# Kernel optimization log

Hardware: AMD Instinct MI355X
Metric: run time of the kernel (lower is better)

## Reference

```python
import jax, jax.numpy as jnp
import numpy as np

COST_CLASS = 1.0
COST_MASK = 1.0
COST_DICE = 1.0


def setup_inputs() -> dict:
    key = jax.random.key(0)
    k1, k2, k3, k4 = jax.random.split(key, 4)
    B, Q, T, H, W, C = 4, 100, 20, 128, 128, 80
    out_probs = jax.random.normal(k1, (B, Q, C), dtype=jnp.float32)
    out_masks = jax.random.uniform(k2, (B, Q, H, W), dtype=jnp.float32)
    target_masks = jax.random.uniform(k3, (B, T, H, W), dtype=jnp.float32)
    target_labels = jax.random.randint(k4, (B, T), 0, C, dtype=jnp.int64)
    return {"out_probs": out_probs, "out_masks": out_masks,
            "target_masks": target_masks, "target_labels": target_labels}


def reference(out_probs, out_masks, target_masks, target_labels):
    # out_probs: [B,Q,C]; out_masks: [B,Q,H,W]; target_masks: [B,T,H,W]; target_labels: [B,T]
    B, Q = out_probs.shape[:2]
    T = target_labels.shape[1]

    # Classification cost: -softmax(out_probs)[b, q, target_labels[b, t]] -> [B,Q,T]
    prob = jax.nn.softmax(out_probs, axis=-1)
    idx = jnp.broadcast_to(target_labels[:, None, :], (B, Q, T))
    cost_class = -jnp.take_along_axis(prob, idx, axis=2)

    out_flat = out_masks.reshape(B, Q, -1)      # [B,Q,HW]
    tgt_flat = target_masks.reshape(B, T, -1)   # [B,T,HW]

    # Pairwise L1 cost over pixels: [B,Q,T]
    cost_mask = jnp.abs(out_flat[:, :, None, :] - tgt_flat[:, None, :, :]).sum(-1)

    # Pairwise dice cost: numerator via batched matmul, sums broadcast.
    inter = jnp.einsum('bqn,btn->bqt', out_flat, tgt_flat)
    denom = out_flat.sum(-1)[:, :, None] + tgt_flat.sum(-1)[:, None, :]
    cost_dice = 1.0 - (2.0 * inter + 1.0) / (denom + 1.0)

    C_mat = COST_MASK * cost_mask + COST_CLASS * cost_class + COST_DICE * cost_dice
    return C_mat  # [B,Q,T] cost matrix (Hungarian assignment runs on CPU outside)
```

## Files before the change

### kernel.cpp

```cpp
#include <hip/hip_runtime.h>
#include <hip/hip_bf16.h>
#include <math.h>

#define B_ 4
#define Q_ 100
#define T_ 20
#define C_ 80
#define HW_ 16384

#define S_ 8
#define QP_ (Q_ / 2)
#define SEG4_ (HW_ / S_ / 4)
#define NIT_ (SEG4_ / 64)
#define TW_ 5

#define NBLK_ (B_ * QP_ * S_)
#define WL_OFF 0
#define WI_OFF (NBLK_ * 40)
#define OS_OFF (WI_OFF + NBLK_ * 40)
#define GS_OFF (OS_OFF + NBLK_ * 2)

typedef float f32x4 __attribute__((ext_vector_type(4)));

__device__ __forceinline__ float wred(float v) {
    v += __shfl_down(v, 32);
    v += __shfl_down(v, 16);
    v += __shfl_down(v, 8);
    v += __shfl_down(v, 4);
    v += __shfl_down(v, 2);
    v += __shfl_down(v, 1);
    return v;
}

template <bool WITH_G>
__device__ __forceinline__ void partial_body(const f32x4* __restrict__ o4,
                                             const f32x4* __restrict__ g4,
                                             float* __restrict__ ws,
                                             int blin, int b, int seg,
                                             int lane, int ts) {
    const int t0 = ts * TW_;

    float accL[2][TW_], accI[2][TW_], os[2], gs[TW_];
#pragma unroll
    for (int qi = 0; qi < 2; ++qi) {
        os[qi] = 0.f;
#pragma unroll
        for (int tj = 0; tj < TW_; ++tj) { accL[qi][tj] = 0.f; accI[qi][tj] = 0.f; }
    }
#pragma unroll
    for (int tj = 0; tj < TW_; ++tj) gs[tj] = 0.f;

#pragma unroll
    for (int it = 0; it < NIT_; ++it) {
        const int ofs = it * 64;
        const f32x4 o0 = o4[ofs];
        const f32x4 o1 = o4[(HW_ / 4) + ofs];
        os[0] += (o0.x + o0.y) + (o0.z + o0.w);
        os[1] += (o1.x + o1.y) + (o1.z + o1.w);
#pragma unroll
        for (int tj = 0; tj < TW_; ++tj) {
            const f32x4 g = g4[(size_t)(t0 + tj) * (HW_ / 4) + ofs];
            if (WITH_G) gs[tj] += (g.x + g.y) + (g.z + g.w);
            accL[0][tj] += (fabsf(o0.x - g.x) + fabsf(o0.y - g.y)) +
                           (fabsf(o0.z - g.z) + fabsf(o0.w - g.w));
            accI[0][tj] = fmaf(o0.x, g.x, accI[0][tj]);
            accI[0][tj] = fmaf(o0.y, g.y, accI[0][tj]);
            accI[0][tj] = fmaf(o0.z, g.z, accI[0][tj]);
            accI[0][tj] = fmaf(o0.w, g.w, accI[0][tj]);
            accL[1][tj] += (fabsf(o1.x - g.x) + fabsf(o1.y - g.y)) +
                           (fabsf(o1.z - g.z) + fabsf(o1.w - g.w));
            accI[1][tj] = fmaf(o1.x, g.x, accI[1][tj]);
            accI[1][tj] = fmaf(o1.y, g.y, accI[1][tj]);
            accI[1][tj] = fmaf(o1.z, g.z, accI[1][tj]);
            accI[1][tj] = fmaf(o1.w, g.w, accI[1][tj]);
        }
    }

    float* WL = ws + WL_OFF;
    float* WI = ws + WI_OFF;
    float* OS = ws + OS_OFF;
    float* GS = ws + GS_OFF;
#pragma unroll
    for (int qi = 0; qi < 2; ++qi) {
#pragma unroll
        for (int tj = 0; tj < TW_; ++tj) {
            const float vL = wred(accL[qi][tj]);
            const float vI = wred(accI[qi][tj]);
            if (lane == 0) {
                WL[(blin * 4 + ts) * 10 + qi * TW_ + tj] = vL;
                WI[(blin * 4 + ts) * 10 + qi * TW_ + tj] = vI;
            }
        }
        const float vo = wred(os[qi]);
        if (ts == 0 && lane == 0) OS[blin * 2 + qi] = vo;
    }
    if (WITH_G) {
#pragma unroll
        for (int tj = 0; tj < TW_; ++tj) {
            const float vg = wred(gs[tj]);
            if (lane == 0) GS[(b * S_ + seg) * T_ + t0 + tj] = vg;
        }
    }
}

__global__ __launch_bounds__(256) void partial_kernel(const float* __restrict__ outm,
                                                      const float* __restrict__ tgtm,
                                                      float* __restrict__ ws) {
    const int r = blockIdx.x & 7;
    const int m = blockIdx.x >> 3;
    const int b = r >> 1;
    const int l = m * 2 + (r & 1);
    const int qp = l >> 3;
    const int seg = l & (S_ - 1);
    const int blin = (b * QP_ + qp) * S_ + seg;

    const int lane = threadIdx.x & 63;
    const int ts   = threadIdx.x >> 6;

    const f32x4* o4 = (const f32x4*)(outm + ((size_t)b * Q_ + qp * 2) * HW_) + seg * SEG4_ + lane;
    const f32x4* g4 = (const f32x4*)(tgtm + (size_t)b * T_ * HW_) + seg * SEG4_ + lane;

    if (qp == 0) partial_body<true>(o4, g4, ws, blin, b, seg, lane, ts);
    else         partial_body<false>(o4, g4, ws, blin, b, seg, lane, ts);
}

__global__ __launch_bounds__(64) void finalize_kernel(const float* __restrict__ probs,
                                                      const int*   __restrict__ labels,
                                                      const float* __restrict__ ws,
                                                      float* __restrict__ out) {
    const int bq = blockIdx.x;
    const int b = bq / Q_;
    const int q = bq % Q_;
    const int qp = q >> 1;
    const int qi = q & 1;

    __shared__ float s_logit[C_];
    for (int c = threadIdx.x; c < C_; c += 64)
        s_logit[c] = probs[(size_t)bq * C_ + c];
    __syncthreads();

    const float* WL = ws + WL_OFF;
    const float* WI = ws + WI_OFF;
    const float* OS = ws + OS_OFF;
    const float* GS = ws + GS_OFF;

    const int t = threadIdx.x;
    if (t < T_) {
        const int ts = t / TW_, tj = t % TW_;
        float L = 0.f, I = 0.f, osum = 0.f, tsum = 0.f;
#pragma unroll
        for (int seg = 0; seg < S_; ++seg) {
            const int blin = (b * QP_ + qp) * S_ + seg;
            L    += WL[(blin * 4 + ts) * 10 + qi * TW_ + tj];
            I    += WI[(blin * 4 + ts) * 10 + qi * TW_ + tj];
            osum += OS[blin * 2 + qi];
            tsum += GS[(b * S_ + seg) * T_ + t];
        }
        float mx = -INFINITY;
#pragma unroll
        for (int c = 0; c < C_; ++c) mx = fmaxf(mx, s_logit[c]);
        float sum = 0.f;
#pragma unroll
        for (int c = 0; c < C_; ++c) sum += __expf(s_logit[c] - mx);
        const int lab = labels[b * T_ + t];
        const float p = __expf(s_logit[lab] - mx) / sum;

        const float denom = osum + tsum;
        const float dice = 1.f - (2.f * I + 1.f) / (denom + 1.f);

        out[(size_t)bq * T_ + t] = L - p + dice;
    }
}

extern "C" void kernel_launch(void* const* d_in, const int* in_sizes, int n_in,
                              void* d_out, int out_size, void* d_ws, size_t ws_size,
                              hipStream_t stream) {
    const float* out_probs     = (const float*)d_in[0];
    const float* out_masks     = (const float*)d_in[1];
    const float* target_masks  = (const float*)d_in[2];
    const int*   target_labels = (const int*)d_in[3];
    float* out = (float*)d_out;

    float* partials = (float*)d_ws;

    partial_kernel<<<B_ * QP_ * S_, 256, 0, stream>>>(out_masks, target_masks, partials);
    finalize_kernel<<<B_ * Q_, 64, 0, stream>>>(out_probs, target_labels, partials, out);
}
```

Measured before the change: 35.60 us.

## Widen query tile to ten per block and shorten cross-lane reductions

Each block now processes 10 queries against 5 targets per wave instead of 2, so every loaded target vector is reused across more queries. The pixel range is split into 16 segments rather than 8, giving 640 blocks instead of 1600. Warp reductions stop at 4 lanes, and the finalize kernel adds the 4 partials per cell with float4 loads. The aim is to cut redundant target-mask reads and reduction shuffles. The cost is far more accumulator registers (about 100 floats plus 15 loaded vectors), which risks lower occupancy or spills, and fewer blocks to spread across the GPU.

New measurement: 62.94 us. 1.77x slower.

```diff
diff --git a/kernel.cpp b/kernel.cpp
--- a/kernel.cpp
+++ b/kernel.cpp
@@ -8,41 +8,38 @@
 #define C_ 80
 #define HW_ 16384
 
-#define S_ 8
-#define QP_ (Q_ / 2)
+#define S_ 16
+#define QG_ 10
+#define NQG_ (Q_ / QG_)
+#define TW_ 5
 #define SEG4_ (HW_ / S_ / 4)
 #define NIT_ (SEG4_ / 64)
-#define TW_ 5
 
-#define NBLK_ (B_ * QP_ * S_)
-#define WL_OFF 0
-#define WI_OFF (NBLK_ * 40)
-#define OS_OFF (WI_OFF + NBLK_ * 40)
-#define GS_OFF (OS_OFF + NBLK_ * 2)
+#define CELL_ 1640
+#define NCELL_ (B_ * NQG_ * S_)
+#define GS_OFF ((size_t)NCELL_ * CELL_)
 
 typedef float f32x4 __attribute__((ext_vector_type(4)));
 
-__device__ __forceinline__ float wred(float v) {
+__device__ __forceinline__ float wred4(float v) {
     v += __shfl_down(v, 32);
     v += __shfl_down(v, 16);
     v += __shfl_down(v, 8);
     v += __shfl_down(v, 4);
-    v += __shfl_down(v, 2);
-    v += __shfl_down(v, 1);
     return v;
 }
 
 template <bool WITH_G>
 __device__ __forceinline__ void partial_body(const f32x4* __restrict__ o4,
                                              const f32x4* __restrict__ g4,
-                                             float* __restrict__ ws,
-                                             int blin, int b, int seg,
+                                             float* __restrict__ rec,
+                                             float* __restrict__ grec,
                                              int lane, int ts) {
     const int t0 = ts * TW_;
 
-    float accL[2][TW_], accI[2][TW_], os[2], gs[TW_];
+    float accL[QG_][TW_], accI[QG_][TW_], os[QG_], gs[TW_];
 #pragma unroll
-    for (int qi = 0; qi < 2; ++qi) {
+    for (int qi = 0; qi < QG_; ++qi) {
         os[qi] = 0.f;
 #pragma unroll
         for (int tj = 0; tj < TW_; ++tj) { accL[qi][tj] = 0.f; accI[qi][tj] = 0.f; }
@@ -53,52 +50,61 @@
 #pragma unroll
     for (int it = 0; it < NIT_; ++it) {
         const int ofs = it * 64;
-        const f32x4 o0 = o4[ofs];
-        const f32x4 o1 = o4[(HW_ / 4) + ofs];
-        os[0] += (o0.x + o0.y) + (o0.z + o0.w);
-        os[1] += (o1.x + o1.y) + (o1.z + o1.w);
+        f32x4 o[QG_];
+#pragma unroll
+        for (int qi = 0; qi < QG_; ++qi) o[qi] = o4[(size_t)qi * (HW_ / 4) + ofs];
+        f32x4 g[TW_];
+#pragma unroll
+        for (int tj = 0; tj < TW_; ++tj) g[tj] = g4[(size_t)(t0 + tj) * (HW_ / 4) + ofs];
+
+        if (ts == 0) {
+#pragma unroll
+            for (int qi = 0; qi < QG_; ++qi)
+                os[qi] += (o[qi].x + o[qi].y) + (o[qi].z + o[qi].w);
+        }
+        if (WITH_G) {
+#pragma unroll
+            for (int tj = 0; tj < TW_; ++tj)
+                gs[tj] += (g[tj].x + g[tj].y) + (g[tj].z + g[tj].w);
+        }
 #pragma unroll
         for (int tj = 0; tj < TW_; ++tj) {
-            const f32x4 g = g4[(size_t)(t0 + tj) * (HW_ / 4) + ofs];
-            if (WITH_G) gs[tj] += (g.x + g.y) + (g.z + g.w);
-            accL[0][tj] += (fabsf(o0.x - g.x) + fabsf(o0.y - g.y)) +
-                           (fabsf(o0.z - g.z) + fabsf(o0.w - g.w));
-            accI[0][tj] = fmaf(o0.x, g.x, accI[0][tj]);
-            accI[0][tj] = fmaf(o0.y, g.y, accI[0][tj]);
-            accI[0][tj] = fmaf(o0.z, g.z, accI[0][tj]);
-            accI[0][tj] = fmaf(o0.w, g.w, accI[0][tj]);
-            accL[1][tj] += (fabsf(o1.x - g.x) + fabsf(o1.y - g.y)) +
-                           (fabsf(o1.z - g.z) + fabsf(o1.w - g.w));
-            accI[1][tj] = fmaf(o1.x, g.x, accI[1][tj]);
-            accI[1][tj] = fmaf(o1.y, g.y, accI[1][tj]);
-            accI[1][tj] = fmaf(o1.z, g.z, accI[1][tj]);
-            accI[1][tj] = fmaf(o1.w, g.w, accI[1][tj]);
+#pragma unroll
+            for (int qi = 0; qi < QG_; ++qi) {
+                accL[qi][tj] += (fabsf(o[qi].x - g[tj].x) + fabsf(o[qi].y - g[tj].y)) +
+                                (fabsf(o[qi].z - g[tj].z) + fabsf(o[qi].w - g[tj].w));
+                accI[qi][tj] = fmaf(o[qi].x, g[tj].x, accI[qi][tj]);
+                accI[qi][tj] = fmaf(o[qi].y, g[tj].y, accI[qi][tj]);
+                accI[qi][tj] = fmaf(o[qi].z, g[tj].z, accI[qi][tj]);
+                accI[qi][tj] = fmaf(o[qi].w, g[tj].w, accI[qi][tj]);
+            }
         }
     }
 
-    float* WL = ws + WL_OFF;
-    float* WI = ws + WI_OFF;
-    float* OS = ws + OS_OFF;
-    float* GS = ws + GS_OFF;
 #pragma unroll
-    for (int qi = 0; qi < 2; ++qi) {
+    for (int qi = 0; qi < QG_; ++qi) {
 #pragma unroll
         for (int tj = 0; tj < TW_; ++tj) {
-            const float vL = wred(accL[qi][tj]);
-            const float vI = wred(accI[qi][tj]);
-            if (lane == 0) {
-                WL[(blin * 4 + ts) * 10 + qi * TW_ + tj] = vL;
-                WI[(blin * 4 + ts) * 10 + qi * TW_ + tj] = vI;
+            const float vL = wred4(accL[qi][tj]);
+            const float vI = wred4(accI[qi][tj]);
+            if (lane < 4) {
+                rec[(qi * T_ + t0 + tj) * 4 + lane]       = vL;
+                rec[800 + (qi * T_ + t0 + tj) * 4 + lane] = vI;
             }
         }
-        const float vo = wred(os[qi]);
-        if (ts == 0 && lane == 0) OS[blin * 2 + qi] = vo;
+    }
+    if (ts == 0) {
+#pragma unroll
+        for (int qi = 0; qi < QG_; ++qi) {
+            const float vo = wred4(os[qi]);
+            if (lane < 4) rec[1600 + qi * 4 + lane] = vo;
+        }
     }
     if (WITH_G) {
 #pragma unroll
         for (int tj = 0; tj < TW_; ++tj) {
-            const float vg = wred(gs[tj]);
-            if (lane == 0) GS[(b * S_ + seg) * T_ + t0 + tj] = vg;
+            const float vg = wred4(gs[tj]);
+            if (lane < 4) grec[(t0 + tj) * 4 + lane] = vg;
         }
     }
 }
@@ -110,18 +116,19 @@
     const int m = blockIdx.x >> 3;
     const int b = r >> 1;
     const int l = m * 2 + (r & 1);
-    const int qp = l >> 3;
+    const int qg = l >> 4;
     const int seg = l & (S_ - 1);
-    const int blin = (b * QP_ + qp) * S_ + seg;
 
     const int lane = threadIdx.x & 63;
     const int ts   = threadIdx.x >> 6;
 
-    const f32x4* o4 = (const f32x4*)(outm + ((size_t)b * Q_ + qp * 2) * HW_) + seg * SEG4_ + lane;
+    const f32x4* o4 = (const f32x4*)(outm + ((size_t)b * Q_ + qg * QG_) * HW_) + seg * SEG4_ + lane;
     const f32x4* g4 = (const f32x4*)(tgtm + (size_t)b * T_ * HW_) + seg * SEG4_ + lane;
+    float* rec  = ws + ((size_t)(b * NQG_ + qg) * S_ + seg) * CELL_;
+    float* grec = ws + GS_OFF + (size_t)(b * S_ + seg) * T_ * 4;
 
-    if (qp == 0) partial_body<true>(o4, g4, ws, blin, b, seg, lane, ts);
-    else         partial_body<false>(o4, g4, ws, blin, b, seg, lane, ts);
+    if (qg == 0) partial_body<true>(o4, g4, rec, grec, lane, ts);
+    else         partial_body<false>(o4, g4, rec, grec, lane, ts);
 }
 
 __global__ __launch_bounds__(64) void finalize_kernel(const float* __restrict__ probs,
@@ -131,30 +138,29 @@
     const int bq = blockIdx.x;
     const int b = bq / Q_;
     const int q = bq % Q_;
-    const int qp = q >> 1;
-    const int qi = q & 1;
+    const int qg = q / QG_;
+    const int qi = q % QG_;
 
     __shared__ float s_logit[C_];
     for (int c = threadIdx.x; c < C_; c += 64)
         s_logit[c] = probs[(size_t)bq * C_ + c];
     __syncthreads();
 
-    const float* WL = ws + WL_OFF;
-    const float* WI = ws + WI_OFF;
-    const float* OS = ws + OS_OFF;
-    const float* GS = ws + GS_OFF;
-
     const int t = threadIdx.x;
     if (t < T_) {
-        const int ts = t / TW_, tj = t % TW_;
         float L = 0.f, I = 0.f, osum = 0.f, tsum = 0.f;
 #pragma unroll
         for (int seg = 0; seg < S_; ++seg) {
-            const int blin = (b * QP_ + qp) * S_ + seg;
-            L    += WL[(blin * 4 + ts) * 10 + qi * TW_ + tj];
-            I    += WI[(blin * 4 + ts) * 10 + qi * TW_ + tj];
-            osum += OS[blin * 2 + qi];
-            tsum += GS[(b * S_ + seg) * T_ + t];
+            const float4* r4 = (const float4*)(ws + ((size_t)(b * NQG_ + qg) * S_ + seg) * CELL_);
+            const float4* d4 = (const float4*)(ws + GS_OFF + (size_t)(b * S_ + seg) * T_ * 4);
+            const float4 a = r4[qi * T_ + t];
+            const float4 v = r4[200 + qi * T_ + t];
+            const float4 c = r4[400 + qi];
+            const float4 d = d4[t];
+            L    += (a.x + a.y) + (a.z + a.w);
+            I    += (v.x + v.y) + (v.z + v.w);
+            osum += (c.x + c.y) + (c.z + c.w);
+            tsum += (d.x + d.y) + (d.z + d.w);
         }
         float mx = -INFINITY;
 #pragma unroll
@@ -183,6 +189,6 @@
 
     float* partials = (float*)d_ws;
 
-    partial_kernel<<<B_ * QP_ * S_, 256, 0, stream>>>(out_masks, target_masks, partials);
+    partial_kernel<<<B_ * NQG_ * S_, 256, 0, stream>>>(out_masks, target_masks, partials);
     finalize_kernel<<<B_ * Q_, 64, 0, stream>>>(out_probs, target_labels, partials, out);
 }
```
